# Kernel tuning notes

Hardware: AMD Instinct MI355X
Metric: run time of the kernel (lower is better)

Reference implementation:

```python
import jax, jax.numpy as jnp
import numpy as np
from jax.ops import segment_sum

N = 100000
E = 1600000
F_IN = 128
H = 128
C = 40


def setup_inputs() -> dict:
    key = jax.random.key(0)
    k1, k2, k3, k4, k5, k6, k7 = jax.random.split(key, 7)
    row = jax.random.randint(k1, (E,), 0, N)
    col = jax.random.randint(k2, (E,), 0, N)
    edge_index = jnp.stack([row, col]).astype(jnp.int64)
    features = jax.random.normal(k3, (N, F_IN), dtype=jnp.float32)
    W1 = jax.random.normal(k4, (F_IN, H), dtype=jnp.float32) * 0.05
    b1 = jax.random.normal(k5, (H,), dtype=jnp.float32) * 0.05
    W2 = jax.random.normal(k6, (H, C), dtype=jnp.float32) * 0.05
    b2 = jax.random.normal(k7, (C,), dtype=jnp.float32) * 0.05
    return {"edge_index": edge_index, "features": features,
            "W1": W1, "b1": b1, "W2": W2, "b2": b2}


def reference(edge_index, features, W1, b1, W2, b2):
    n = features.shape[0]
    row, col = edge_index[0], edge_index[1]
    # deg of (I + A): 1 (self loop) + row-sum of A
    deg = 1.0 + segment_sum(jnp.ones_like(row, dtype=features.dtype), row,
                            num_segments=n)
    d_inv_sqrt = jnp.where(deg > 0, jax.lax.rsqrt(deg), 0.0)
    edge_w = d_inv_sqrt[row] * d_inv_sqrt[col]          # [E]
    self_w = d_inv_sqrt * d_inv_sqrt                    # [N]

    def spmm(x):
        # adj_normalized @ x, adj_normalized = D^-1/2 (I + A) D^-1/2
        msg = edge_w[:, None] * x[col]                  # [E, F]
        return segment_sum(msg, row, num_segments=n) + self_w[:, None] * x

    x = jax.nn.relu(spmm(features) @ W1 + b1)           # conv1 + relu
    x = spmm(x) @ W2 + b2                               # conv2
    return jnp.mean(x, axis=0)                          # dgl.mean_nodes readout
```

## Files before the change

### kernel.cpp

```cpp
#include <hip/hip_runtime.h>
#include <hip/hip_fp8.h>

#define F 128
#define COUT 40
#define BSH 8
#define CAP 6144
#define CH 8192
#define EPT 16
#define NBLK 512
#define CPAD 32

typedef unsigned int  u32;
typedef unsigned short u16;
typedef __attribute__((ext_vector_type(8))) short short8;
typedef __attribute__((ext_vector_type(4))) float f32x4;

__device__ inline u32 bf16_rne(float f) {
  u32 u = __float_as_uint(f);
  u += 0x7FFFu + ((u >> 16) & 1u);
  return u >> 16;
}

#if defined(__has_builtin)
#if __has_builtin(__builtin_amdgcn_cvt_pk_fp8_f32) && __has_builtin(__builtin_amdgcn_cvt_f32_fp8)
#define HAS_FP8_BUILTIN 1
#endif
#endif

__device__ inline u32 fp8_pk4(float4 a) {
#ifdef HAS_FP8_BUILTIN
  u32 v = (u32)__builtin_amdgcn_cvt_pk_fp8_f32(a.x, a.y, 0, false);
  v = (u32)__builtin_amdgcn_cvt_pk_fp8_f32(a.z, a.w, (int)v, true);
  return v;
#else
  __hip_fp8x2_e4m3 lo(float2{a.x, a.y});
  __hip_fp8x2_e4m3 hi(float2{a.z, a.w});
  return (u32)lo.__x | ((u32)hi.__x << 16);
#endif
}

__device__ inline float2 fp8_dec2(u32 v) {
#ifdef HAS_FP8_BUILTIN
  return make_float2(__builtin_amdgcn_cvt_f32_fp8(v, 0),
                     __builtin_amdgcn_cvt_f32_fp8(v, 1));
#else
  __hip_fp8x2_e4m3 p;
  p.__x = (__hip_fp8x2_storage_t)(v & 0xFFFFu);
  float2 f = (float2)p;
  return make_float2(f.x, f.y);
#endif
}

__global__ void k_zero(int* __restrict__ bcountP, int* __restrict__ bcount2P, int n) {
  int i = blockIdx.x * blockDim.x + threadIdx.x;
  if (i < n) { bcountP[i] = 0; bcount2P[i] = 0; }
}

__global__ void __launch_bounds__(512) k_fat1(
    const int* __restrict__ row, const int* __restrict__ col, int E,
    int* __restrict__ bcountP, unsigned* __restrict__ staging,
    int* __restrict__ bcount2P, unsigned* __restrict__ staging2,
    int nbuck, int nbB,
    const float4* __restrict__ X, uint2* __restrict__ Xq, int nvec,
    const float* __restrict__ W1, u16* __restrict__ W1T) {
  __shared__ u32 pay1[CH];
  __shared__ u32 pay2[CH];
  __shared__ int hist1[512];
  __shared__ int hist2[512];
  __shared__ int lcur1[512];
  __shared__ int lcur2[512];
  __shared__ int gdelta1[512];
  __shared__ int gdelta2[512];
  int b = blockIdx.x;
  int t = threadIdx.x;

  if (b < nbB) {
    int base = b * CH;
    int n = E - base; if (n > CH) n = CH;
    int r[EPT], c[EPT];
#pragma unroll
    for (int j = 0; j < EPT; ++j) {
      int i = t + j * 512;
      if (i < n) { r[j] = row[base + i]; c[j] = col[base + i]; }
      else       { r[j] = -1; c[j] = -1; }
    }
    hist1[t] = 0; hist2[t] = 0;
    __syncthreads();
#pragma unroll
    for (int j = 0; j < EPT; ++j) if (r[j] >= 0) {
      atomicAdd(&hist1[r[j] >> BSH], 1);
      atomicAdd(&hist2[c[j] >> BSH], 1);
    }
    __syncthreads();
    int h1 = hist1[t], h2 = hist2[t];
    for (int off = 1; off < 512; off <<= 1) {
      int x1 = hist1[t], x2 = hist2[t];
      int y1 = (t >= off) ? hist1[t - off] : 0;
      int y2 = (t >= off) ? hist2[t - off] : 0;
      __syncthreads();
      hist1[t] = x1 + y1; hist2[t] = x2 + y2;
      __syncthreads();
    }
    if (t < nbuck) {
      int e1 = hist1[t] - h1, e2 = hist2[t] - h2;
      int s1 = (h1 > 0) ? atomicAdd(&bcountP[t * CPAD], h1) : 0;
      int s2 = (h2 > 0) ? atomicAdd(&bcount2P[t * CPAD], h2) : 0;
      gdelta1[t] = t * CAP + s1 - e1;
      gdelta2[t] = t * CAP + s2 - e2;
      lcur1[t] = e1; lcur2[t] = e2;
    }
    __syncthreads();
#pragma unroll
    for (int j = 0; j < EPT; ++j) if (r[j] >= 0) {
      int bk = r[j] >> BSH;
      int s = atomicAdd(&lcur1[bk], 1);
      pay1[s] = ((u32)(bk & 127) << 25) | ((u32)(r[j] & 255) << 17) | (u32)c[j];
      int bk2 = c[j] >> BSH;
      int s2 = atomicAdd(&lcur2[bk2], 1);
      pay2[s2] = ((u32)(bk2 & 127) << 25) | ((u32)(c[j] & 255) << 17) | (u32)r[j];
    }
    __syncthreads();
    int q1a = hist1[127], q1b = hist1[255], q1c = hist1[383];
    int q2a = hist2[127], q2b = hist2[255], q2c = hist2[383];
#pragma unroll
    for (int j = 0; j < EPT; ++j) {
      int i = t + j * 512;
      if (i < n) {
        u32 p = pay1[i];
        int bk = (((i >= q1a) + (i >= q1b) + (i >= q1c)) << 7) | (int)(p >> 25);
        int dst = i + gdelta1[bk];
        if (dst < (bk + 1) * CAP) staging[dst] = p;
        u32 p2 = pay2[i];
        int bk2 = (((i >= q2a) + (i >= q2b) + (i >= q2c)) << 7) | (int)(p2 >> 25);
        int dst2 = i + gdelta2[bk2];
        if (dst2 < (bk2 + 1) * CAP) staging2[dst2] = p2;
      }
    }
  } else if (b < nbB + 32) {
    int i = (b - nbB) * 512 + t;
    int k = i >> 7, nn = i & 127;
    W1T[nn * 128 + k] = (u16)bf16_rne(W1[i]);
  } else {
    int i = (b - nbB - 32) * 512 + t;
    if (i < nvec) {
      float4 a = X[2 * i], v = X[2 * i + 1];
      uint2 o;
      o.x = fp8_pk4(a);
      o.y = fp8_pk4(v);
      Xq[i] = o;
    }
  }
}

__global__ void __launch_bounds__(1024) k_build(
    const unsigned* __restrict__ staging,
    const int* __restrict__ bcountP,
    int2* __restrict__ rpd, float* __restrict__ dis,
    int* __restrict__ csr, int N) {
  __shared__ int cnt[256];
  __shared__ int cur[256];
  __shared__ u32 srt[CAP];
  int b = blockIdx.x;
  int t = threadIdx.x;
  int r0 = b << BSH;
  int nrows = N - r0; if (nrows > 256) nrows = 256;
  int ecnt = bcountP[b * CPAD]; if (ecnt > CAP) ecnt = CAP;
  const unsigned* sg = staging + (size_t)b * CAP;
  int gb = b * CAP;

  if (t < 256) cnt[t] = 0;
  __syncthreads();
  for (int i = t; i < ecnt; i += 1024) atomicAdd(&cnt[(sg[i] >> 17) & 255], 1);
  __syncthreads();
  int d = (t < 256) ? cnt[t] : 0;
  for (int off = 1; off < 256; off <<= 1) {
    int x = 0, y = 0;
    if (t < 256) { x = cnt[t]; y = (t >= off) ? cnt[t - off] : 0; }
    __syncthreads();
    if (t < 256) cnt[t] = x + y;
    __syncthreads();
  }
  if (t < 256) {
    int excl = cnt[t] - d;
    if (t < nrows) {
      rpd[r0 + t] = make_int2(gb + excl, d);
      dis[r0 + t] = rsqrtf(1.0f + (float)d);
    }
    cur[t] = excl;
  }
  __syncthreads();
  for (int i = t; i < ecnt; i += 1024) {
    unsigned p = sg[i];
    int j = atomicAdd(&cur[(p >> 17) & 255], 1);
    srt[j] = p & 0x1FFFFu;
  }
  __syncthreads();
  for (int i = t; i < ecnt; i += 1024)
    csr[gb + i] = (int)srt[i];
}

__global__ void __launch_bounds__(256) k_spmm(
    const u16* __restrict__ Xq,
    const int2* __restrict__ rpd,
    const float* __restrict__ dis,
    const int* __restrict__ csr,
    u16* __restrict__ z1h, int N,
    const unsigned* __restrict__ staging2,
    const int* __restrict__ bcount2P,
    float* __restrict__ tcol, int nbuck) {
  __shared__ float lacc[256];
  int blk = blockIdx.x;
  int t = threadIdx.x;

  if (blk < nbuck) {
    lacc[t] = 0.f;
    __syncthreads();
    int ecnt = bcount2P[blk * CPAD]; if (ecnt > CAP) ecnt = CAP;
    const unsigned* sg = staging2 + (size_t)blk * CAP;
    for (int i = t; i < ecnt; i += 256) {
      unsigned p = sg[i];
      int lc = (p >> 17) & 255;
      int r = (int)(p & 0x1FFFFu);
      atomicAdd(&lacc[lc], dis[r]);
    }
    __syncthreads();
    int c = (blk << BSH) + t;
    if (c < N) tcol[c] = lacc[t];
    return;
  }

  int wid = ((blk - nbuck) * 256 + t) >> 6;
  int rowi = __builtin_amdgcn_readfirstlane(wid);
  if (rowi >= N) return;
  int lane = t & 63;
  float dr = dis[rowi];
  u32 sv = Xq[(size_t)rowi * 64 + lane];
  float2 acc = make_float2(0.f, 0.f);
  int2 rd = rpd[rowi];
  int e0 = rd.x, e1 = rd.x + rd.y;
  int e = e0;
  for (; e + 16 <= e1; e += 16) {
    int c[16]; u32 v[16]; float w[16];
#pragma unroll
    for (int j = 0; j < 16; ++j) c[j] = csr[e + j];
#pragma unroll
    for (int j = 0; j < 16; ++j) v[j] = Xq[(size_t)c[j] * 64 + lane];
#pragma unroll
    for (int j = 0; j < 16; ++j) w[j] = dis[c[j]];
#pragma unroll
    for (int j = 0; j < 16; ++j) {
      float2 xv = fp8_dec2(v[j]);
      acc.x += w[j] * xv.x;
      acc.y += w[j] * xv.y;
    }
  }
  for (; e + 4 <= e1; e += 4) {
    int c[4]; u32 v[4]; float w[4];
#pragma unroll
    for (int j = 0; j < 4; ++j) c[j] = csr[e + j];
#pragma unroll
    for (int j = 0; j < 4; ++j) v[j] = Xq[(size_t)c[j] * 64 + lane];
#pragma unroll
    for (int j = 0; j < 4; ++j) w[j] = dis[c[j]];
#pragma unroll
    for (int j = 0; j < 4; ++j) {
      float2 xv = fp8_dec2(v[j]);
      acc.x += w[j] * xv.x;
      acc.y += w[j] * xv.y;
    }
  }
  for (; e < e1; ++e) {
    int c = csr[e];
    float w = dis[c];
    float2 xv = fp8_dec2(Xq[(size_t)c * 64 + lane]);
    acc.x += w * xv.x;
    acc.y += w * xv.y;
  }
  float2 sf = fp8_dec2(sv);
  acc.x = dr * (acc.x + dr * sf.x);
  acc.y = dr * (acc.y + dr * sf.y);
  ((u32*)(z1h + (size_t)rowi * F))[lane] = bf16_rne(acc.x) | (bf16_rne(acc.y) << 16);
}

__global__ void __launch_bounds__(256) k_gemm_red(
    const u16* __restrict__ z1h,
    const u16* __restrict__ W1T,
    const float* __restrict__ b1,
    const float* __restrict__ dis,
    const float* __restrict__ tcol,
    float* __restrict__ partials, int N, int ntiles) {
  __shared__ float smat[16][128];
  int t = threadIdx.x;
  int w = t >> 6;
  int l = t & 63;
  int lr = l & 15;
  int lg = l >> 4;
  const u16* bbase = W1T + (size_t)lr * 128 + lg * 8;

  float psum[8] = {};

  for (int tile = blockIdx.x; tile < ntiles; tile += gridDim.x) {
    int g0 = tile * 64;
    int garow = g0 + 16 * w + lr;
    if (garow >= N) garow = N - 1;
    const u16* arow = z1h + (size_t)garow * F + lg * 8;
    short8 afr[4];
#pragma unroll
    for (int kb = 0; kb < 4; ++kb)
      afr[kb] = *(const short8*)(arow + kb * 32);

    float cw[4];
#pragma unroll
    for (int j = 0; j < 4; ++j) {
      int g = g0 + 16 * w + lg * 4 + j;
      float c = 0.f;
      if (g < N) { float d = dis[g]; c = d * (d + tcol[g]); }
      cw[j] = c;
    }

#pragma unroll
    for (int n = 0; n < 8; ++n) {
      f32x4 acc = {0.f, 0.f, 0.f, 0.f};
      const u16* bp = bbase + (size_t)(16 * n) * 128;
#pragma unroll
      for (int kb = 0; kb < 4; ++kb) {
        short8 bfr = *(const short8*)(bp + kb * 32);
        acc = __builtin_amdgcn_mfma_f32_16x16x32_bf16(afr[kb], bfr, acc, 0, 0, 0);
      }
      float bb = b1[16 * n + lr];
      float p = 0.f;
#pragma unroll
      for (int j = 0; j < 4; ++j) {
        float h = acc[j] + bb;
        h = h > 0.f ? h : 0.f;
        p += cw[j] * h;
      }
      psum[n] += p;
    }
  }

#pragma unroll
  for (int n = 0; n < 8; ++n) smat[4 * w + lg][16 * n + lr] = psum[n];
  __syncthreads();
  if (t < F) {
    float v = 0.f;
#pragma unroll
    for (int i = 0; i < 16; ++i) v += smat[i][t];
    partials[blockIdx.x * F + t] = v;
  }
}

__global__ void k_finish(const float* __restrict__ partials, int nblk,
                         const float* __restrict__ W2, const float* __restrict__ b2,
                         float* __restrict__ out, float invN) {
  __shared__ float sl[F];
  int t = threadIdx.x;
  float v = 0.f;
#pragma unroll 8
  for (int b = 0; b < nblk; ++b) v += partials[b * F + t];
  sl[t] = v * invN;
  __syncthreads();
  if (t < COUT) {
    float acc = b2[t];
#pragma unroll
    for (int k = 0; k < F; ++k) acc += sl[k] * W2[k * COUT + t];
    out[t] = acc;
  }
}

extern "C" void kernel_launch(void* const* d_in, const int* in_sizes, int n_in,
                              void* d_out, int out_size, void* d_ws, size_t ws_size,
                              hipStream_t stream) {
  const int* edge = (const int*)d_in[0];
  const float* X  = (const float*)d_in[1];
  const float* W1 = (const float*)d_in[2];
  const float* b1 = (const float*)d_in[3];
  const float* W2 = (const float*)d_in[4];
  const float* b2 = (const float*)d_in[5];
  float* out = (float*)d_out;

  int E = in_sizes[0] / 2;
  int N = in_sizes[1] / F;
  const int* row = edge;
  const int* col = edge + E;
  int nbuck = (N + 255) >> BSH;
  int ntiles = (N + 63) / 64;
  int nbB = (E + CH - 1) / CH;
  int nvec = (N * F) / 8;
  int ncast = (nvec + 511) / 512;

  char* w = (char*)d_ws;
  auto alloc = [&](size_t bytes) {
    char* p = w;
    w += (bytes + 255) & ~(size_t)255;
    return p;
  };
  float*    tcol     = (float*)alloc((size_t)N * 4);
  float*    dis      = (float*)alloc((size_t)N * 4);
  int2*     rpd      = (int2*)alloc((size_t)N * 8);
  float*    partials = (float*)alloc((size_t)NBLK * F * 4);
  int*      bcountP  = (int*)alloc((size_t)512 * CPAD * 4);
  int*      bcount2P = (int*)alloc((size_t)512 * CPAD * 4);
  u16*      Xq       = (u16*)alloc((size_t)N * F);
  u16*      W1T      = (u16*)alloc((size_t)F * F * 2);
  unsigned* staging  = (unsigned*)alloc((size_t)nbuck * CAP * 4);
  unsigned* staging2 = (unsigned*)alloc((size_t)nbuck * CAP * 4);
  int*      csr      = (int*)alloc((size_t)nbuck * CAP * 4);
  u16*      z1h      = (u16*)alloc((size_t)N * F * 2);

  int nzero = 512 * CPAD;

  k_zero  <<<(nzero + 255) / 256, 256, 0, stream>>>(bcountP, bcount2P, nzero);
  k_fat1  <<<nbB + 32 + ncast, 512, 0, stream>>>(row, col, E, bcountP, staging,
                                                 bcount2P, staging2, nbuck, nbB,
                                                 (const float4*)X, (uint2*)Xq, nvec,
                                                 W1, W1T);
  k_build <<<nbuck, 1024, 0, stream>>>(staging, bcountP, rpd, dis, csr, N);
  k_spmm  <<<nbuck + (N + 3) / 4, 256, 0, stream>>>(Xq, rpd, dis, csr, z1h, N,
                                                    staging2, bcount2P, tcol, nbuck);
  k_gemm_red<<<NBLK, 256, 0, stream>>>(z1h, W1T, b1, dis, tcol, partials, N, ntiles);
  k_finish<<<1, 128, 0, stream>>>(partials, NBLK, W2, b2, out, 1.0f / (float)N);
}
```

Before: 132.6 us.

## Fuse CSR build into SpMM using LDS-resident sorted edge buckets

Splits the old build kernel into a small degree kernel and merges the per-bucket counting sort into the SpMM kernel. Each 1024-thread block keeps its 256-row bucket's sorted column indices in shared memory and gathers neighbour features directly, so the global csr and rpd arrays are no longer written and re-read. The cost is a recount of degrees in two kernels, large LDS use per block that limits occupancy, and far fewer, coarser blocks (one per 256 rows), which can hurt load balance and latency hiding for the gather.

```diff
diff --git a/kernel.cpp b/kernel.cpp
--- a/kernel.cpp
+++ b/kernel.cpp
@@ -152,21 +152,65 @@
   }
 }
 
-__global__ void __launch_bounds__(1024) k_build(
+__global__ void __launch_bounds__(1024) k_deg(
     const unsigned* __restrict__ staging,
     const int* __restrict__ bcountP,
-    int2* __restrict__ rpd, float* __restrict__ dis,
-    int* __restrict__ csr, int N) {
+    float* __restrict__ dis, int N) {
+  __shared__ int cnt[256];
+  int b = blockIdx.x;
+  int t = threadIdx.x;
+  int ecnt = bcountP[b * CPAD]; if (ecnt > CAP) ecnt = CAP;
+  const unsigned* sg = staging + (size_t)b * CAP;
+  if (t < 256) cnt[t] = 0;
+  __syncthreads();
+  for (int i = t; i < ecnt; i += 1024) atomicAdd(&cnt[(sg[i] >> 17) & 255], 1);
+  __syncthreads();
+  if (t < 256) {
+    int g = (b << BSH) + t;
+    if (g < N) dis[g] = rsqrtf(1.0f + (float)cnt[t]);
+  }
+}
+
+__global__ void __launch_bounds__(1024) k_spmm(
+    const u16* __restrict__ Xq,
+    const float* __restrict__ dis,
+    const unsigned* __restrict__ staging,
+    const int* __restrict__ bcountP,
+    u16* __restrict__ z1h, int N,
+    const unsigned* __restrict__ staging2,
+    const int* __restrict__ bcount2P,
+    float* __restrict__ tcol, int nbuck) {
+  __shared__ u32 srt[CAP];
   __shared__ int cnt[256];
   __shared__ int cur[256];
-  __shared__ u32 srt[CAP];
-  int b = blockIdx.x;
+  __shared__ int degl[256];
+  __shared__ float disl[256];
+  __shared__ float lacc[256];
+  int blk = blockIdx.x;
   int t = threadIdx.x;
+
+  if (blk >= nbuck) {
+    int b = blk - nbuck;
+    if (t < 256) lacc[t] = 0.f;
+    __syncthreads();
+    int ecnt = bcount2P[b * CPAD]; if (ecnt > CAP) ecnt = CAP;
+    const unsigned* sg = staging2 + (size_t)b * CAP;
+    for (int i = t; i < ecnt; i += 1024) {
+      unsigned p = sg[i];
+      atomicAdd(&lacc[(p >> 17) & 255], dis[p & 0x1FFFFu]);
+    }
+    __syncthreads();
+    if (t < 256) {
+      int c = (b << BSH) + t;
+      if (c < N) tcol[c] = lacc[t];
+    }
+    return;
+  }
+
+  int b = blk;
   int r0 = b << BSH;
-  int nrows = N - r0; if (nrows > 256) nrows = 256;
   int ecnt = bcountP[b * CPAD]; if (ecnt > CAP) ecnt = CAP;
   const unsigned* sg = staging + (size_t)b * CAP;
-  int gb = b * CAP;
 
   if (t < 256) cnt[t] = 0;
   __syncthreads();
@@ -181,12 +225,9 @@
     __syncthreads();
   }
   if (t < 256) {
-    int excl = cnt[t] - d;
-    if (t < nrows) {
-      rpd[r0 + t] = make_int2(gb + excl, d);
-      dis[r0 + t] = rsqrtf(1.0f + (float)d);
-    }
-    cur[t] = excl;
+    degl[t] = d;
+    disl[t] = rsqrtf(1.0f + (float)d);
+    cur[t] = cnt[t] - d;
   }
   __syncthreads();
   for (int i = t; i < ecnt; i += 1024) {
@@ -195,91 +236,46 @@
     srt[j] = p & 0x1FFFFu;
   }
   __syncthreads();
-  for (int i = t; i < ecnt; i += 1024)
-    csr[gb + i] = (int)srt[i];
-}
-
-__global__ void __launch_bounds__(256) k_spmm(
-    const u16* __restrict__ Xq,
-    const int2* __restrict__ rpd,
-    const float* __restrict__ dis,
-    const int* __restrict__ csr,
-    u16* __restrict__ z1h, int N,
-    const unsigned* __restrict__ staging2,
-    const int* __restrict__ bcount2P,
-    float* __restrict__ tcol, int nbuck) {
-  __shared__ float lacc[256];
-  int blk = blockIdx.x;
-  int t = threadIdx.x;
-
-  if (blk < nbuck) {
-    lacc[t] = 0.f;
-    __syncthreads();
-    int ecnt = bcount2P[blk * CPAD]; if (ecnt > CAP) ecnt = CAP;
-    const unsigned* sg = staging2 + (size_t)blk * CAP;
-    for (int i = t; i < ecnt; i += 256) {
-      unsigned p = sg[i];
-      int lc = (p >> 17) & 255;
-      int r = (int)(p & 0x1FFFFu);
-      atomicAdd(&lacc[lc], dis[r]);
-    }
-    __syncthreads();
-    int c = (blk << BSH) + t;
-    if (c < N) tcol[c] = lacc[t];
-    return;
-  }
-
-  int wid = ((blk - nbuck) * 256 + t) >> 6;
-  int rowi = __builtin_amdgcn_readfirstlane(wid);
-  if (rowi >= N) return;
+
+  int w = t >> 6;
   int lane = t & 63;
-  float dr = dis[rowi];
-  u32 sv = Xq[(size_t)rowi * 64 + lane];
-  float2 acc = make_float2(0.f, 0.f);
-  int2 rd = rpd[rowi];
-  int e0 = rd.x, e1 = rd.x + rd.y;
-  int e = e0;
-  for (; e + 16 <= e1; e += 16) {
-    int c[16]; u32 v[16]; float w[16];
-#pragma unroll
-    for (int j = 0; j < 16; ++j) c[j] = csr[e + j];
-#pragma unroll
-    for (int j = 0; j < 16; ++j) v[j] = Xq[(size_t)c[j] * 64 + lane];
-#pragma unroll
-    for (int j = 0; j < 16; ++j) w[j] = dis[c[j]];
-#pragma unroll
-    for (int j = 0; j < 16; ++j) {
-      float2 xv = fp8_dec2(v[j]);
-      acc.x += w[j] * xv.x;
-      acc.y += w[j] * xv.y;
-    }
-  }
-  for (; e + 4 <= e1; e += 4) {
-    int c[4]; u32 v[4]; float w[4];
-#pragma unroll
-    for (int j = 0; j < 4; ++j) c[j] = csr[e + j];
-#pragma unroll
-    for (int j = 0; j < 4; ++j) v[j] = Xq[(size_t)c[j] * 64 + lane];
-#pragma unroll
-    for (int j = 0; j < 4; ++j) w[j] = dis[c[j]];
-#pragma unroll
-    for (int j = 0; j < 4; ++j) {
-      float2 xv = fp8_dec2(v[j]);
-      acc.x += w[j] * xv.x;
-      acc.y += w[j] * xv.y;
-    }
-  }
-  for (; e < e1; ++e) {
-    int c = csr[e];
-    float w = dis[c];
-    float2 xv = fp8_dec2(Xq[(size_t)c * 64 + lane]);
-    acc.x += w * xv.x;
-    acc.y += w * xv.y;
-  }
-  float2 sf = fp8_dec2(sv);
-  acc.x = dr * (acc.x + dr * sf.x);
-  acc.y = dr * (acc.y + dr * sf.y);
-  ((u32*)(z1h + (size_t)rowi * F))[lane] = bf16_rne(acc.x) | (bf16_rne(acc.y) << 16);
+  for (int rr = w; rr < 256; rr += 16) {
+    int grow = r0 + rr;
+    if (grow >= N) continue;
+    int deg = degl[rr];
+    int e0 = cnt[rr] - deg;
+    float dr = disl[rr];
+    u32 sv = Xq[(size_t)grow * 64 + lane];
+    float2 acc = make_float2(0.f, 0.f);
+    int e = e0, e1 = e0 + deg;
+    for (; e + 8 <= e1; e += 8) {
+      int c[8]; u32 v[8]; float wt[8];
+#pragma unroll
+      for (int j = 0; j < 8; ++j)
+        c[j] = __builtin_amdgcn_readfirstlane((int)srt[e + j]);
+#pragma unroll
+      for (int j = 0; j < 8; ++j) v[j] = Xq[(size_t)c[j] * 64 + lane];
+#pragma unroll
+      for (int j = 0; j < 8; ++j) wt[j] = dis[c[j]];
+#pragma unroll
+      for (int j = 0; j < 8; ++j) {
+        float2 xv = fp8_dec2(v[j]);
+        acc.x += wt[j] * xv.x;
+        acc.y += wt[j] * xv.y;
+      }
+    }
+    for (; e < e1; ++e) {
+      int c = __builtin_amdgcn_readfirstlane((int)srt[e]);
+      float wt = dis[c];
+      float2 xv = fp8_dec2(Xq[(size_t)c * 64 + lane]);
+      acc.x += wt * xv.x;
+      acc.y += wt * xv.y;
+    }
+    float2 sf = fp8_dec2(sv);
+    acc.x = dr * (acc.x + dr * sf.x);
+    acc.y = dr * (acc.y + dr * sf.y);
+    ((u32*)(z1h + (size_t)grow * F))[lane] = bf16_rne(acc.x) | (bf16_rne(acc.y) << 16);
+  }
 }
 
 __global__ void __launch_bounds__(256) k_gemm_red(
@@ -314,7 +310,7 @@
     for (int j = 0; j < 4; ++j) {
       int g = g0 + 16 * w + lg * 4 + j;
       float c = 0.f;
-      if (g < N) { float d = dis[g]; c = d * (d + tcol[g]); }
+      if (g < N) { float dv = dis[g]; c = dv * (dv + tcol[g]); }
       cw[j] = c;
     }
 
@@ -397,7 +393,6 @@
   };
   float*    tcol     = (float*)alloc((size_t)N * 4);
   float*    dis      = (float*)alloc((size_t)N * 4);
-  int2*     rpd      = (int2*)alloc((size_t)N * 8);
   float*    partials = (float*)alloc((size_t)NBLK * F * 4);
   int*      bcountP  = (int*)alloc((size_t)512 * CPAD * 4);
   int*      bcount2P = (int*)alloc((size_t)512 * CPAD * 4);
@@ -405,7 +400,6 @@
   u16*      W1T      = (u16*)alloc((size_t)F * F * 2);
   unsigned* staging  = (unsigned*)alloc((size_t)nbuck * CAP * 4);
   unsigned* staging2 = (unsigned*)alloc((size_t)nbuck * CAP * 4);
-  int*      csr      = (int*)alloc((size_t)nbuck * CAP * 4);
   u16*      z1h      = (u16*)alloc((size_t)N * F * 2);
 
   int nzero = 512 * CPAD;
@@ -415,9 +409,9 @@
                                                  bcount2P, staging2, nbuck, nbB,
                                                  (const float4*)X, (uint2*)Xq, nvec,
                                                  W1, W1T);
-  k_build <<<nbuck, 1024, 0, stream>>>(staging, bcountP, rpd, dis, csr, N);
-  k_spmm  <<<nbuck + (N + 3) / 4, 256, 0, stream>>>(Xq, rpd, dis, csr, z1h, N,
-                                                    staging2, bcount2P, tcol, nbuck);
+  k_deg   <<<nbuck, 1024, 0, stream>>>(staging, bcountP, dis, N);
+  k_spmm  <<<2 * nbuck, 1024, 0, stream>>>(Xq, dis, staging, bcountP, z1h, N,
+                                           staging2, bcount2P, tcol, nbuck);
   k_gemm_red<<<NBLK, 256, 0, stream>>>(z1h, W1T, b1, dis, tcol, partials, N, ntiles);
   k_finish<<<1, 128, 0, stream>>>(partials, NBLK, W2, b2, out, 1.0f / (float)N);
 }
```

Result: slower. 137.5 us (+3.7%).
